# Kernel tuning notes

Measured on AMD Instinct MI355X. Metric: run time of the kernel, lower is better.

## Reference

```python
import jax, jax.numpy as jnp
import numpy as np
from jax import lax

B, S, I, H = 32, 512, 768, 256
STD = 0.02


def setup_inputs() -> dict:
    key = jax.random.key(0)
    ks = jax.random.split(key, 12)
    nrm = lambda k, shp: STD * jax.random.normal(k, shp, dtype=jnp.float32)
    return {
        "inputs": jax.random.normal(ks[0], (B, S, I), dtype=jnp.float32),
        "times": jax.random.uniform(ks[1], (B, S, 1), dtype=jnp.float32),
        "Wi": nrm(ks[2], (I, H)), "Ui": nrm(ks[3], (H, H)), "bi": jnp.zeros((H,), jnp.float32),
        "Wf": nrm(ks[4], (I, H)), "Uf": nrm(ks[5], (H, H)), "bf": jnp.zeros((H,), jnp.float32),
        "Wog": nrm(ks[6], (I, H)), "Uog": nrm(ks[7], (H, H)), "bog": jnp.zeros((H,), jnp.float32),
        "Wc": nrm(ks[8], (I, H)), "Uc": nrm(ks[9], (H, H)), "bc": jnp.zeros((H,), jnp.float32),
        "W_decomp": nrm(ks[10], (H, H)), "b_decomp": jnp.zeros((H,), jnp.float32),
    }


def _tlstm(inputs, times, Wi, Ui, bi, Wf, Uf, bf, Wog, Uog, bog, Wc, Uc, bc, W_decomp, b_decomp):
    # inputs: [B,S,I], times: [B,S,1] -> time-major [S,B,*]
    x = jnp.transpose(inputs, (1, 0, 2))  # [S,B,I]
    t = jnp.transpose(times, (1, 0, 2))   # [S,B,1]
    b, h = inputs.shape[0], Wi.shape[1]
    h0 = jnp.zeros((b, h), inputs.dtype)
    e_const = jnp.asarray(np.e, inputs.dtype)

    def step(carry, xt):
        hs, cs = carry
        xi, ti = xt
        T = 1.0 / jnp.log(ti + e_const)                    # [B,1], broadcasts over H
        C_ST = jnp.tanh(cs @ W_decomp + b_decomp)
        cs = cs - C_ST + T * C_ST                          # time-decayed cell
        i = jax.nn.sigmoid(xi @ Wi + hs @ Ui + bi)
        f = jax.nn.sigmoid(xi @ Wf + hs @ Uf + bf)
        o = jax.nn.sigmoid(xi @ Wog + hs @ Uog + bog)
        Cc = jax.nn.sigmoid(xi @ Wc + hs @ Uc + bc)        # NOTE: sigmoid (as in source), not tanh
        ct = f * cs + i * Cc
        ht = o * jnp.tanh(ct)
        return (ht, ct), ht

    (h_f, c_f), his_f = lax.scan(step, (h0, h0), (x, t))
    # backward direction: inputs flipped; time sequence is [t_0, t_{S-1}, ..., t_1]
    xb = x[::-1]
    tb = jnp.concatenate([t[:1], t[:0:-1]], axis=0)
    (h_b, c_b), his_b = lax.scan(step, (h0, h0), (xb, tb))

    hidden_his = jnp.concatenate([his_f, his_b], axis=2)   # [S,B,2H]
    hidden_his = jnp.transpose(hidden_his, (1, 0, 2))      # [B,S,2H]
    h_last = jnp.concatenate([h_f, h_b], axis=1)
    c_last = jnp.concatenate([c_f, c_b], axis=1)
    return hidden_his, (h_last, c_last)


def reference(inputs, times, Wi, Ui, bi, Wf, Uf, bf, Wog, Uog, bog, Wc, Uc, bc, W_decomp, b_decomp):
    return _tlstm(inputs, times, Wi, Ui, bi, Wf, Uf, bf, Wog, Uog, bog, Wc, Uc, bc, W_decomp, b_decomp)
```

## Files before the change

### kernel.cpp

```cpp
#include <hip/hip_runtime.h>
#include <math.h>

#define SLEN 512
#define BATCH 32
#define IDIM 768
#define HDIM 256
#define NDIM 1024

typedef unsigned short u16;
typedef unsigned int u32;
typedef unsigned long long u64;
typedef __attribute__((ext_vector_type(8))) short short8;
typedef __attribute__((ext_vector_type(4))) float float4v;
typedef __attribute__((ext_vector_type(4))) unsigned short ushort4v;
typedef __attribute__((ext_vector_type(4))) unsigned int uint4v;

__device__ __forceinline__ float bf2f(u16 v) {
    union { u32 u; float f; } c; c.u = ((u32)v) << 16; return c.f;
}
__device__ __forceinline__ u16 f2bf(float f) {
    union { float f; u32 u; } c; c.f = f;
    u32 u = c.u;
    return (u16)((u + 0x7fffu + ((u >> 16) & 1u)) >> 16);
}
__device__ __forceinline__ float sigm(float x) { return 1.f / (1.f + __expf(-x)); }
__device__ __forceinline__ float tanh_f(float x) { return 1.f - 2.f / (__expf(2.f * x) + 1.f); }

struct WPtrs {
    const float *Wi, *Ui, *bi, *Wf, *Uf, *bfp, *Wog, *Uog, *bog, *Wc, *Uc, *bc, *Wd, *bd;
};

__global__ void convert_kernel(WPtrs p, u16* __restrict__ W4t, u16* __restrict__ U4t,
                               float* __restrict__ b4) {
    const float* Wg[4] = {p.Wi, p.Wf, p.Wog, p.Wc};
    const float* Ug[4] = {p.Ui, p.Uf, p.Uog, p.Uc};
    const float* bg[4] = {p.bi, p.bfp, p.bog, p.bc};
    const int total = NDIM * IDIM + 5 * HDIM * HDIM + NDIM;
    for (int idx = blockIdx.x * blockDim.x + threadIdx.x; idx < total;
         idx += gridDim.x * blockDim.x) {
        int i = idx;
        if (i < NDIM * IDIM) {
            int n = i / IDIM, k = i - n * IDIM;
            W4t[i] = f2bf(Wg[n >> 8][k * HDIM + (n & 255)]);
        } else if ((i -= NDIM * IDIM) < 5 * HDIM * HDIM) {
            int g = i >> 16, rem = i & 65535, n = rem >> 8, k = rem & 255;
            const float* M = (g < 4) ? Ug[g] : p.Wd;
            U4t[i] = f2bf(M[k * HDIM + n]);
        } else {
            i -= 5 * HDIM * HDIM;
            b4[i] = bg[i >> 8][i & 255];
        }
    }
}

__global__ __launch_bounds__(256) void gemm_g_kernel(const float* __restrict__ x,
                                                     const u16* __restrict__ W4t,
                                                     const float* __restrict__ b4,
                                                     u16* __restrict__ G) {
    __shared__ u16 As[128][40];
    __shared__ u16 Bs[128][40];
    const int bn = blockIdx.x;
    const int bm = blockIdx.y;
    const int tid = threadIdx.x;
    const int w = tid >> 6, lane = tid & 63;
    const int wr = w >> 1, wc = w & 1;
    const int l15 = lane & 15, quad = lane >> 4;
    const int m0 = bm * 128, n0 = bn * 128;

    float4v acc[4][4];
#pragma unroll
    for (int a = 0; a < 4; ++a)
#pragma unroll
        for (int b = 0; b < 4; ++b) acc[a][b] = (float4v)(0.f);

    for (int kt = 0; kt < IDIM / 32; ++kt) {
        const int k0 = kt * 32;
#pragma unroll
        for (int i = 0; i < 4; ++i) {
            int idx = tid + 256 * i;
            int r = idx >> 3, seg = idx & 7;
            float4v xv = *(const float4v*)(x + (size_t)(m0 + r) * IDIM + k0 + seg * 4);
            ushort4v t;
            t.x = f2bf(xv.x); t.y = f2bf(xv.y); t.z = f2bf(xv.z); t.w = f2bf(xv.w);
            *(ushort4v*)(&As[r][seg * 4]) = t;
        }
#pragma unroll
        for (int i = 0; i < 2; ++i) {
            int idx = tid + 256 * i;
            int r = idx >> 2, seg = idx & 3;
            uint4v bv = *(const uint4v*)(W4t + (size_t)(n0 + r) * IDIM + k0 + seg * 8);
            *(uint4v*)(&Bs[r][seg * 8]) = bv;
        }
        __syncthreads();
        short8 afr[4], bfr[4];
#pragma unroll
        for (int mt = 0; mt < 4; ++mt) {
            int row = wr * 64 + mt * 16 + l15;
            afr[mt] = *(const short8*)(&As[row][quad * 8]);
        }
#pragma unroll
        for (int nt = 0; nt < 4; ++nt) {
            int col = wc * 64 + nt * 16 + l15;
            bfr[nt] = *(const short8*)(&Bs[col][quad * 8]);
        }
#pragma unroll
        for (int mt = 0; mt < 4; ++mt)
#pragma unroll
            for (int nt = 0; nt < 4; ++nt)
                acc[mt][nt] = __builtin_amdgcn_mfma_f32_16x16x32_bf16(afr[mt], bfr[nt],
                                                                      acc[mt][nt], 0, 0, 0);
        __syncthreads();
    }
#pragma unroll
    for (int mt = 0; mt < 4; ++mt)
#pragma unroll
        for (int nt = 0; nt < 4; ++nt) {
            int gm = m0 + wr * 64 + mt * 16 + quad * 4;
            int gn = n0 + wc * 64 + nt * 16 + l15;
            float bias = b4[gn];
#pragma unroll
            for (int r = 0; r < 4; ++r) {
                G[(size_t)(gm + r) * NDIM + gn] = f2bf(acc[mt][nt][r] + bias);
            }
        }
}

__global__ __launch_bounds__(256, 1) void recur_mfma_kernel(
    const float* __restrict__ times, const float* __restrict__ bd,
    const u16* __restrict__ U4t, const u16* __restrict__ G,
    u64* __restrict__ exch, float* __restrict__ out) {
    __shared__ u16 hL[32 * 264];
    __shared__ u16 cL[32 * 264];
    const int d = blockIdx.x >> 2;
    const int slice = blockIdx.x & 3;
    const int tid = threadIdx.x;
    const int w = tid >> 6;
    const int lane = tid & 63;
    const int l15 = lane & 15;
    const int quad = lane >> 4;
    const int j = slice * 64 + w * 16 + l15;
    const float bdec = bd[j];

    short8 Bf[5][8];
#pragma unroll
    for (int g = 0; g < 5; ++g)
#pragma unroll
        for (int q = 0; q < 8; ++q)
            Bf[g][q] = *(const short8*)(U4t + (g << 16) + (j << 8) + (q << 5) + (quad << 3));

    float creg[2][4], hreg[2][4];
#pragma unroll
    for (int mt = 0; mt < 2; ++mt)
#pragma unroll
        for (int r = 0; r < 4; ++r) { creg[mt][r] = 0.f; hreg[mt][r] = 0.f; }

    for (int s = 0; s < SLEN; ++s) {
        const int sf = d ? (SLEN - 1 - s) : s;
        const int tt = d ? (s == 0 ? 0 : SLEN - s) : s;

        float4v acc[5][2];
#pragma unroll
        for (int g = 0; g < 4; ++g)
#pragma unroll
            for (int mt = 0; mt < 2; ++mt) {
                const u16* Gp = G + (size_t)((mt * 16 + quad * 4) * SLEN + sf) * NDIM + g * 256 + j;
                float4v a;
#pragma unroll
                for (int r = 0; r < 4; ++r) a[r] = bf2f(Gp[(size_t)r * SLEN * NDIM]);
                acc[g][mt] = a;
            }
        float Tv[2][4];
#pragma unroll
        for (int mt = 0; mt < 2; ++mt)
#pragma unroll
            for (int r = 0; r < 4; ++r) {
                const int b = mt * 16 + quad * 4 + r;
                Tv[mt][r] = 1.f / logf(times[b * SLEN + tt] + 2.718281828459045f);
            }
#pragma unroll
        for (int mt = 0; mt < 2; ++mt) acc[4][mt] = (float4v)(bdec);

        if (s > 0) {
            const u64* ex = exch + ((size_t)((d << 1) | ((s - 1) & 1)) << 13);
            u64 vals[32];
            bool ok = false;
            while (!ok) {
                ok = true;
#pragma unroll
                for (int i = 0; i < 32; ++i)
                    vals[i] = __hip_atomic_load(&ex[(i << 8) | tid], __ATOMIC_RELAXED,
                                                __HIP_MEMORY_SCOPE_AGENT);
#pragma unroll
                for (int i = 0; i < 32; ++i)
                    ok = ok && ((u32)vals[i] == (u32)(s - 1));
            }
#pragma unroll
            for (int i = 0; i < 32; ++i) {
                u32 hi = (u32)(vals[i] >> 32);
                hL[i * 264 + tid] = (u16)(hi & 0xffffu);
                cL[i * 264 + tid] = (u16)(hi >> 16);
            }
            __syncthreads();

            short8 Ah[2][8], Ac[2][8];
#pragma unroll
            for (int mt = 0; mt < 2; ++mt)
#pragma unroll
                for (int q = 0; q < 8; ++q) {
                    const int off = (mt * 16 + l15) * 264 + q * 32 + quad * 8;
                    Ah[mt][q] = *(const short8*)(hL + off);
                    Ac[mt][q] = *(const short8*)(cL + off);
                }
#pragma unroll
            for (int q = 0; q < 8; ++q)
#pragma unroll
                for (int mt = 0; mt < 2; ++mt) {
                    acc[0][mt] = __builtin_amdgcn_mfma_f32_16x16x32_bf16(Ah[mt][q], Bf[0][q], acc[0][mt], 0, 0, 0);
                    acc[1][mt] = __builtin_amdgcn_mfma_f32_16x16x32_bf16(Ah[mt][q], Bf[1][q], acc[1][mt], 0, 0, 0);
                    acc[2][mt] = __builtin_amdgcn_mfma_f32_16x16x32_bf16(Ah[mt][q], Bf[2][q], acc[2][mt], 0, 0, 0);
                    acc[3][mt] = __builtin_amdgcn_mfma_f32_16x16x32_bf16(Ah[mt][q], Bf[3][q], acc[3][mt], 0, 0, 0);
                    acc[4][mt] = __builtin_amdgcn_mfma_f32_16x16x32_bf16(Ac[mt][q], Bf[4][q], acc[4][mt], 0, 0, 0);
                }
            __syncthreads();
        }

        u64* exw = exch + ((size_t)((d << 1) | (s & 1)) << 13);
#pragma unroll
        for (int mt = 0; mt < 2; ++mt)
#pragma unroll
            for (int r = 0; r < 4; ++r) {
                const int b = mt * 16 + quad * 4 + r;
                const float C_ST = tanh_f(acc[4][mt][r]);
                const float cs = creg[mt][r] - C_ST + Tv[mt][r] * C_ST;
                const float ig = sigm(acc[0][mt][r]);
                const float fg = sigm(acc[1][mt][r]);
                const float og = sigm(acc[2][mt][r]);
                const float Cc = sigm(acc[3][mt][r]);
                const float cn = fg * cs + ig * Cc;
                const float hn = og * tanh_f(cn);
                creg[mt][r] = cn;
                hreg[mt][r] = hn;
                const u32 payload = ((u32)f2bf(cn) << 16) | (u32)f2bf(hn);
                const u64 v = ((u64)payload << 32) | (u32)s;
                __hip_atomic_store(&exw[(b << 8) | j], v, __ATOMIC_RELAXED,
                                   __HIP_MEMORY_SCOPE_AGENT);
                out[((size_t)b * SLEN + s) * 512 + d * 256 + j] = hn;
            }
    }

    const size_t base2 = (size_t)BATCH * SLEN * 512;
#pragma unroll
    for (int mt = 0; mt < 2; ++mt)
#pragma unroll
        for (int r = 0; r < 4; ++r) {
            const int b = mt * 16 + quad * 4 + r;
            out[base2 + b * 512 + d * 256 + j] = hreg[mt][r];
            out[base2 + BATCH * 512 + b * 512 + d * 256 + j] = creg[mt][r];
        }
}

extern "C" void kernel_launch(void* const* d_in, const int* in_sizes, int n_in,
                              void* d_out, int out_size, void* d_ws, size_t ws_size,
                              hipStream_t stream) {
    const float* inputs = (const float*)d_in[0];
    const float* times = (const float*)d_in[1];
    WPtrs p;
    p.Wi = (const float*)d_in[2];  p.Ui = (const float*)d_in[3];  p.bi = (const float*)d_in[4];
    p.Wf = (const float*)d_in[5];  p.Uf = (const float*)d_in[6];  p.bfp = (const float*)d_in[7];
    p.Wog = (const float*)d_in[8]; p.Uog = (const float*)d_in[9]; p.bog = (const float*)d_in[10];
    p.Wc = (const float*)d_in[11]; p.Uc = (const float*)d_in[12]; p.bc = (const float*)d_in[13];
    p.Wd = (const float*)d_in[14]; p.bd = (const float*)d_in[15];

    char* ws = (char*)d_ws;
    u16* W4t = (u16*)ws;
    u16* U4t = (u16*)(ws + 1572864);
    float* b4 = (float*)(ws + 2228224);
    u16* G = (u16*)(ws + 2232320);
    u64* exch = (u64*)ws;

    hipLaunchKernelGGL(convert_kernel, dim3(1024), dim3(256), 0, stream, p, W4t, U4t, b4);
    hipLaunchKernelGGL(gemm_g_kernel, dim3(8, 128), dim3(256), 0, stream, inputs, W4t, b4, G);
    hipMemsetAsync(ws, 0xFF, 262144, stream);
    hipLaunchKernelGGL(recur_mfma_kernel, dim3(8), dim3(256), 0, stream, times, p.bd, U4t, G,
                       exch, (float*)d_out);
}
```

Before: 3.126 ms.

## Split each direction across two blocks and exchange only the remote half

The recurrence now runs on 2 blocks of 512 threads per direction instead of 4 blocks of 256. Each block writes its own half of h/c straight into double-buffered LDS and polls the global exchange buffer only for the other block's half. This cuts the number of blocks each step waits on and the volume of global atomic polling. Double buffering also removes the trailing __syncthreads per step. In exchange, each CU carries more waves and more MFMA work per step, and the recurrence runs on fewer CUs.

Measured after the change: 4.196 ms. +34.2%, slower.

```diff
diff --git a/kernel.cpp b/kernel.cpp
--- a/kernel.cpp
+++ b/kernel.cpp
@@ -125,28 +125,32 @@
         }
 }
 
-__global__ __launch_bounds__(256, 1) void recur_mfma_kernel(
+__global__ __launch_bounds__(512, 2) void recur_mfma_kernel(
     const float* __restrict__ times, const float* __restrict__ bd,
     const u16* __restrict__ U4t, const u16* __restrict__ G,
     u64* __restrict__ exch, float* __restrict__ out) {
-    __shared__ u16 hL[32 * 264];
-    __shared__ u16 cL[32 * 264];
-    const int d = blockIdx.x >> 2;
-    const int slice = blockIdx.x & 3;
+    __shared__ u16 hL[2][32 * 264];
+    __shared__ u16 cL[2][32 * 264];
+    const int d = blockIdx.x >> 1;
+    const int hf = blockIdx.x & 1;
     const int tid = threadIdx.x;
     const int w = tid >> 6;
     const int lane = tid & 63;
     const int l15 = lane & 15;
     const int quad = lane >> 4;
-    const int j = slice * 64 + w * 16 + l15;
-    const float bdec = bd[j];
+    const int J = hf * 128 + w * 16 + l15;
+    const float bdec = bd[J];
+    const int exbaseW = ((d << 2) | (hf ^ 0)) , dummy = exbaseW;
+    (void)dummy;
+    const int pb = tid >> 4;
+    const int pc = (tid & 15) << 3;
 
     short8 Bf[5][8];
 #pragma unroll
     for (int g = 0; g < 5; ++g)
 #pragma unroll
         for (int q = 0; q < 8; ++q)
-            Bf[g][q] = *(const short8*)(U4t + (g << 16) + (j << 8) + (q << 5) + (quad << 3));
+            Bf[g][q] = *(const short8*)(U4t + (g << 16) + (J << 8) + (q << 5) + (quad << 3));
 
     float creg[2][4], hreg[2][4];
 #pragma unroll
@@ -163,7 +167,7 @@
         for (int g = 0; g < 4; ++g)
 #pragma unroll
             for (int mt = 0; mt < 2; ++mt) {
-                const u16* Gp = G + (size_t)((mt * 16 + quad * 4) * SLEN + sf) * NDIM + g * 256 + j;
+                const u16* Gp = G + (size_t)((mt * 16 + quad * 4) * SLEN + sf) * NDIM + g * 256 + J;
                 float4v a;
 #pragma unroll
                 for (int r = 0; r < 4; ++r) a[r] = bf2f(Gp[(size_t)r * SLEN * NDIM]);
@@ -181,25 +185,31 @@
         for (int mt = 0; mt < 2; ++mt) acc[4][mt] = (float4v)(bdec);
 
         if (s > 0) {
-            const u64* ex = exch + ((size_t)((d << 1) | ((s - 1) & 1)) << 13);
-            u64 vals[32];
+            const int rp = (s - 1) & 1;
+            const u64* ex = exch + ((size_t)(((d << 1) | rp) * 2 + (1 - hf)) << 12) +
+                            (pb << 7) + pc;
+            u64 vals[8];
             bool ok = false;
             while (!ok) {
                 ok = true;
 #pragma unroll
-                for (int i = 0; i < 32; ++i)
-                    vals[i] = __hip_atomic_load(&ex[(i << 8) | tid], __ATOMIC_RELAXED,
+                for (int i = 0; i < 8; ++i)
+                    vals[i] = __hip_atomic_load(&ex[i], __ATOMIC_RELAXED,
                                                 __HIP_MEMORY_SCOPE_AGENT);
 #pragma unroll
-                for (int i = 0; i < 32; ++i)
+                for (int i = 0; i < 8; ++i)
                     ok = ok && ((u32)vals[i] == (u32)(s - 1));
             }
-#pragma unroll
-            for (int i = 0; i < 32; ++i) {
+            short8 hv, cv;
+#pragma unroll
+            for (int i = 0; i < 8; ++i) {
                 u32 hi = (u32)(vals[i] >> 32);
-                hL[i * 264 + tid] = (u16)(hi & 0xffffu);
-                cL[i * 264 + tid] = (u16)(hi >> 16);
-            }
+                hv[i] = (short)(u16)(hi & 0xffffu);
+                cv[i] = (short)(u16)(hi >> 16);
+            }
+            const int doff = pb * 264 + (1 - hf) * 128 + pc;
+            *(short8*)(&hL[rp][doff]) = hv;
+            *(short8*)(&cL[rp][doff]) = cv;
             __syncthreads();
 
             short8 Ah[2][8], Ac[2][8];
@@ -208,8 +218,8 @@
 #pragma unroll
                 for (int q = 0; q < 8; ++q) {
                     const int off = (mt * 16 + l15) * 264 + q * 32 + quad * 8;
-                    Ah[mt][q] = *(const short8*)(hL + off);
-                    Ac[mt][q] = *(const short8*)(cL + off);
+                    Ah[mt][q] = *(const short8*)(&hL[rp][off]);
+                    Ac[mt][q] = *(const short8*)(&cL[rp][off]);
                 }
 #pragma unroll
             for (int q = 0; q < 8; ++q)
@@ -221,10 +231,10 @@
                     acc[3][mt] = __builtin_amdgcn_mfma_f32_16x16x32_bf16(Ah[mt][q], Bf[3][q], acc[3][mt], 0, 0, 0);
                     acc[4][mt] = __builtin_amdgcn_mfma_f32_16x16x32_bf16(Ac[mt][q], Bf[4][q], acc[4][mt], 0, 0, 0);
                 }
-            __syncthreads();
-        }
-
-        u64* exw = exch + ((size_t)((d << 1) | (s & 1)) << 13);
+        }
+
+        const int wp = s & 1;
+        u64* exw = exch + ((size_t)(((d << 1) | wp) * 2 + hf) << 12);
 #pragma unroll
         for (int mt = 0; mt < 2; ++mt)
 #pragma unroll
@@ -240,11 +250,14 @@
                 const float hn = og * tanh_f(cn);
                 creg[mt][r] = cn;
                 hreg[mt][r] = hn;
-                const u32 payload = ((u32)f2bf(cn) << 16) | (u32)f2bf(hn);
-                const u64 v = ((u64)payload << 32) | (u32)s;
-                __hip_atomic_store(&exw[(b << 8) | j], v, __ATOMIC_RELAXED,
+                const u16 hb16 = f2bf(hn), cb16 = f2bf(cn);
+                const u32 payload = ((u32)cb16 << 16) | (u32)hb16;
+                __hip_atomic_store(&exw[(b << 7) + (w * 16 + l15)],
+                                   ((u64)payload << 32) | (u32)s, __ATOMIC_RELAXED,
                                    __HIP_MEMORY_SCOPE_AGENT);
-                out[((size_t)b * SLEN + s) * 512 + d * 256 + j] = hn;
+                hL[wp][b * 264 + J] = hb16;
+                cL[wp][b * 264 + J] = cb16;
+                out[((size_t)b * SLEN + s) * 512 + d * 256 + J] = hn;
             }
     }
 
@@ -254,8 +267,8 @@
 #pragma unroll
         for (int r = 0; r < 4; ++r) {
             const int b = mt * 16 + quad * 4 + r;
-            out[base2 + b * 512 + d * 256 + j] = hreg[mt][r];
-            out[base2 + BATCH * 512 + b * 512 + d * 256 + j] = creg[mt][r];
+            out[base2 + b * 512 + d * 256 + J] = hreg[mt][r];
+            out[base2 + BATCH * 512 + b * 512 + d * 256 + J] = creg[mt][r];
         }
 }
 
@@ -280,7 +293,7 @@
 
     hipLaunchKernelGGL(convert_kernel, dim3(1024), dim3(256), 0, stream, p, W4t, U4t, b4);
     hipLaunchKernelGGL(gemm_g_kernel, dim3(8, 128), dim3(256), 0, stream, inputs, W4t, b4, G);
-    hipMemsetAsync(ws, 0xFF, 262144, stream);
-    hipLaunchKernelGGL(recur_mfma_kernel, dim3(8), dim3(256), 0, stream, times, p.bd, U4t, G,
+    hipMemsetAsync(ws, 0xFF, 524288, stream);
+    hipLaunchKernelGGL(recur_mfma_kernel, dim3(4), dim3(512), 0, stream, times, p.bd, U4t, G,
                        exch, (float*)d_out);
 }
```
